# Kernel optimization log

Hardware: AMD Instinct MI355X
Metric: run time of the kernel (lower is better)

The kernel has to match this reference:

```python
import jax, jax.numpy as jnp
import numpy as np

N_GENES = 768
HID = 128


def setup_inputs() -> dict:
    key = jax.random.key(0)
    ks = jax.random.split(key, 7)
    s1 = 1.0 / np.sqrt(2 * HID)
    s2 = 1.0 / np.sqrt(HID)
    return {
        "gene_embeddings": jax.random.normal(ks[0], (N_GENES, HID), jnp.float32),
        # regulatory_classifier: Linear(2h -> h), ReLU, Linear(h -> 3)
        "W1": jax.random.normal(ks[1], (HID, 2 * HID), jnp.float32) * s1,
        "b1": jax.random.normal(ks[2], (HID,), jnp.float32) * s1,
        "W2": jax.random.normal(ks[3], (3, HID), jnp.float32) * s2,
        "b2": jax.random.normal(ks[4], (3,), jnp.float32) * s2,
        # binding_predictor: Bilinear(h, h, 1) -> weight [1, h, h], bias [1]
        "Wb": jax.random.normal(ks[5], (1, HID, HID), jnp.float32) * s2,
        "bb": jax.random.normal(ks[6], (1,), jnp.float32) * s2,
    }


def reference(gene_embeddings, W1, b1, W2, b2, Wb, bb):
    """Vectorized equivalent of GeneRegulatoryNetwork.compute_regulatory_matrix.

    For every ordered pair (i, j), i != j:
      logits   = MLP(cat[x_i, x_j])            -> [3]
      cls      = argmax(logits)
      affinity = x_i^T Wb x_j + bb             (nn.Bilinear, out=1)
      reg[i,j] = +affinity if cls==0, -affinity if cls==2, else 0
    """
    X = gene_embeddings  # [n, h]
    n, h = X.shape
    # Linear(2h -> h) on cat[x_i, x_j] splits into two per-gene projections.
    Ai = X @ W1[:, :h].T  # [n, h] contribution of gene_i
    Bj = X @ W1[:, h:].T  # [n, h] contribution of gene_j
    hidden = jax.nn.relu(Ai[:, None, :] + Bj[None, :, :] + b1)  # [n, n, h]
    logits = hidden @ W2.T + b2  # [n, n, 3]
    reg_class = jnp.argmax(logits, axis=-1)  # [n, n] (first-max, matches torch)
    # Bilinear affinity: x_i^T Wb[0] x_j + bb[0]
    affinity = jnp.einsum('ik,kl,jl->ij', X, Wb[0], X) + bb[0]  # [n, n]
    sign = jnp.where(reg_class == 0, 1.0, jnp.where(reg_class == 2, -1.0, 0.0))
    reg = (sign * affinity).astype(X.dtype)
    # i == j pairs are skipped in the original loop -> zero diagonal
    reg = reg * (1.0 - jnp.eye(n, dtype=reg.dtype))
    return reg
```

## Files before the change

### kernel.cpp

```cpp
#include <hip/hip_runtime.h>

#define N_GENES 768
#define H 128
#define TILE 48
#define LDP 132

__global__ __launch_bounds__(128) void grn_pre(
    const float* __restrict__ X, const float* __restrict__ W1,
    const float* __restrict__ b1, const float* __restrict__ Wb,
    float* __restrict__ AiB, float* __restrict__ Bjp, float* __restrict__ Y)
{
    const int m  = threadIdx.x;
    const int g0 = blockIdx.x * 4;

    __shared__ float Xs[4][H];
    #pragma unroll
    for (int r = 0; r < 4; ++r) Xs[r][m] = X[(g0 + r) * H + m];
    __syncthreads();

    double aib[4] = {0, 0, 0, 0}, bj[4] = {0, 0, 0, 0}, y[4] = {0, 0, 0, 0};
    const float4* W1a = (const float4*)(W1 + m * (2 * H));
    const float4* W1b = (const float4*)(W1 + m * (2 * H) + H);

    #pragma unroll 4
    for (int kq = 0; kq < H / 4; ++kq) {
        float4 wa = W1a[kq];
        float4 wb = W1b[kq];
        float wc[4];
        #pragma unroll
        for (int e = 0; e < 4; ++e) wc[e] = Wb[(kq * 4 + e) * H + m];
        const float* wae = &wa.x;
        const float* wbe = &wb.x;
        #pragma unroll
        for (int r = 0; r < 4; ++r) {
            float4 xr = *(const float4*)&Xs[r][kq * 4];
            const float* xe = &xr.x;
            #pragma unroll
            for (int e = 0; e < 4; ++e) {
                aib[r] += (double)xe[e] * (double)wae[e];
                bj[r]  += (double)xe[e] * (double)wbe[e];
                y[r]   += (double)xe[e] * (double)wc[e];
            }
        }
    }

    const double b1m = (double)b1[m];
    #pragma unroll
    for (int r = 0; r < 4; ++r) {
        AiB[(g0 + r) * H + m] = (float)(aib[r] + b1m);
        Bjp[(g0 + r) * H + m] = (float)bj[r];
        Y  [(g0 + r) * H + m] = (float)y[r];
    }
}

__device__ __forceinline__ void load_tile(float* __restrict__ dst,
                                          const float* __restrict__ src, int tx)
{
    #pragma unroll
    for (int t = 0; t < 6; ++t) {
        int idx = tx + t * 256;
        int row = idx >> 5;
        int c4  = idx & 31;
        *(float4*)&dst[row * LDP + c4 * 4] = *(const float4*)&src[row * H + c4 * 4];
    }
}

__global__ __launch_bounds__(256) void grn_main(
    const float* __restrict__ AiB, const float* __restrict__ Bjp,
    const float* __restrict__ Y,   const float* __restrict__ X,
    const float* __restrict__ W2,  const float* __restrict__ b2,
    const float* __restrict__ bb,  float* __restrict__ out)
{
    const int gj = blockIdx.x & 15;
    const int gi = blockIdx.x >> 4;
    const int tx = threadIdx.x;
    const int it = tx >> 4;
    const int jt = tx & 15;

    __shared__ float sL[TILE * LDP];
    __shared__ float sR[TILE * LDP];
    __shared__ float sW0[H];
    __shared__ float sW1[H];

    load_tile(sL, Y + gi * TILE * H, tx);
    load_tile(sR, X + gj * TILE * H, tx);
    if (tx < H) {
        sW0[tx] = W2[tx] - W2[2 * H + tx];
        sW1[tx] = W2[tx] - W2[H + tx];
    }
    __syncthreads();

    float aff[3][3] = {};
    #pragma unroll 4
    for (int mq = 0; mq < H / 4; ++mq) {
        float4 yv[3], xv[3];
        #pragma unroll
        for (int r = 0; r < 3; ++r) yv[r] = *(const float4*)&sL[(it + 16 * r) * LDP + mq * 4];
        #pragma unroll
        for (int c = 0; c < 3; ++c) xv[c] = *(const float4*)&sR[(jt + 16 * c) * LDP + mq * 4];
        #pragma unroll
        for (int r = 0; r < 3; ++r) {
            const float* ye = &yv[r].x;
            #pragma unroll
            for (int c = 0; c < 3; ++c) {
                const float* xe = &xv[c].x;
                #pragma unroll
                for (int e = 0; e < 4; ++e)
                    aff[r][c] = fmaf(ye[e], xe[e], aff[r][c]);
            }
        }
    }

    __syncthreads();

    load_tile(sL, AiB + gi * TILE * H, tx);
    load_tile(sR, Bjp + gj * TILE * H, tx);
    __syncthreads();

    const float u0 = b2[0] - b2[2];
    const float v0 = b2[0] - b2[1];
    float u[3][3], v[3][3];
    #pragma unroll
    for (int r = 0; r < 3; ++r)
        #pragma unroll
        for (int c = 0; c < 3; ++c) { u[r][c] = u0; v[r][c] = v0; }

    #pragma unroll 4
    for (int mq = 0; mq < H / 4; ++mq) {
        float4 w0 = *(const float4*)&sW0[mq * 4];
        float4 w1 = *(const float4*)&sW1[mq * 4];
        const float* w0e = &w0.x;
        const float* w1e = &w1.x;
        float4 av[3], bv[3];
        #pragma unroll
        for (int r = 0; r < 3; ++r) av[r] = *(const float4*)&sL[(it + 16 * r) * LDP + mq * 4];
        #pragma unroll
        for (int c = 0; c < 3; ++c) bv[c] = *(const float4*)&sR[(jt + 16 * c) * LDP + mq * 4];
        #pragma unroll
        for (int r = 0; r < 3; ++r) {
            const float* ae = &av[r].x;
            #pragma unroll
            for (int c = 0; c < 3; ++c) {
                const float* be = &bv[c].x;
                #pragma unroll
                for (int e = 0; e < 4; ++e) {
                    float h = fmaxf(ae[e] + be[e], 0.0f);
                    u[r][c] = fmaf(h, w0e[e], u[r][c]);
                    v[r][c] = fmaf(h, w1e[e], v[r][c]);
                }
            }
        }
    }

    const float bbv = bb[0];
    #pragma unroll
    for (int r = 0; r < 3; ++r) {
        const int i = gi * TILE + it + 16 * r;
        #pragma unroll
        for (int c = 0; c < 3; ++c) {
            const int j = gj * TILE + jt + 16 * c;
            float A = aff[r][c] + bbv;
            float uu = u[r][c], vv = v[r][c];
            float s = (uu >= 0.0f && vv >= 0.0f) ? A
                    : ((uu < 0.0f && uu < vv) ? -A : 0.0f);
            if (i == j) s = 0.0f;
            out[i * N_GENES + j] = s;
        }
    }
}

extern "C" void kernel_launch(void* const* d_in, const int* in_sizes, int n_in,
                              void* d_out, int out_size, void* d_ws, size_t ws_size,
                              hipStream_t stream)
{
    const float* X  = (const float*)d_in[0];
    const float* W1 = (const float*)d_in[1];
    const float* b1 = (const float*)d_in[2];
    const float* W2 = (const float*)d_in[3];
    const float* b2 = (const float*)d_in[4];
    const float* Wb = (const float*)d_in[5];
    const float* bb = (const float*)d_in[6];
    float* out = (float*)d_out;

    float* ws  = (float*)d_ws;
    float* AiB = ws;
    float* Bjp = ws + N_GENES * H;
    float* Yw  = ws + 2 * N_GENES * H;

    grn_pre <<<N_GENES / 4, 128, 0, stream>>>(X, W1, b1, Wb, AiB, Bjp, Yw);
    grn_main<<<256,         256, 0, stream>>>(AiB, Bjp, Yw, X, W2, b2, bb, out);
}
```

Before: 94.05 us.

## Compute bilinear affinity in fp16 with fdot2 and rebalance pre-kernel grid

The pre-kernel now writes the Y projection and a copy of X as fp16. The main kernel computes the bilinear affinity from these with packed fp16 dot-product instructions (fdot2), which halves the shared-memory and global traffic for that phase. The pre-kernel handles 3 genes per block instead of 4, giving more blocks, and the hidden-layer loop is rewritten with 2-wide vector add/max. The fp16 inputs lose precision in the affinity values, which may push results past the tolerance.

```diff
diff --git a/kernel.cpp b/kernel.cpp
--- a/kernel.cpp
+++ b/kernel.cpp
@@ -4,21 +4,27 @@
 #define H 128
 #define TILE 48
 #define LDP 132
+#define LDPH 136
+
+typedef float    f2 __attribute__((ext_vector_type(2)));
+typedef _Float16 h2 __attribute__((ext_vector_type(2)));
+typedef _Float16 h8 __attribute__((ext_vector_type(8)));
 
 __global__ __launch_bounds__(128) void grn_pre(
     const float* __restrict__ X, const float* __restrict__ W1,
     const float* __restrict__ b1, const float* __restrict__ Wb,
-    float* __restrict__ AiB, float* __restrict__ Bjp, float* __restrict__ Y)
+    float* __restrict__ AiB, float* __restrict__ Bjp,
+    _Float16* __restrict__ Yh, _Float16* __restrict__ Xh)
 {
     const int m  = threadIdx.x;
-    const int g0 = blockIdx.x * 4;
-
-    __shared__ float Xs[4][H];
-    #pragma unroll
-    for (int r = 0; r < 4; ++r) Xs[r][m] = X[(g0 + r) * H + m];
-    __syncthreads();
-
-    double aib[4] = {0, 0, 0, 0}, bj[4] = {0, 0, 0, 0}, y[4] = {0, 0, 0, 0};
+    const int g0 = blockIdx.x * 3;
+
+    __shared__ float Xs[3][H];
+    #pragma unroll
+    for (int r = 0; r < 3; ++r) Xs[r][m] = X[(g0 + r) * H + m];
+    __syncthreads();
+
+    double aib[3] = {0, 0, 0}, bj[3] = {0, 0, 0}, y[3] = {0, 0, 0};
     const float4* W1a = (const float4*)(W1 + m * (2 * H));
     const float4* W1b = (const float4*)(W1 + m * (2 * H) + H);
 
@@ -32,7 +38,7 @@
         const float* wae = &wa.x;
         const float* wbe = &wb.x;
         #pragma unroll
-        for (int r = 0; r < 4; ++r) {
+        for (int r = 0; r < 3; ++r) {
             float4 xr = *(const float4*)&Xs[r][kq * 4];
             const float* xe = &xr.x;
             #pragma unroll
@@ -46,15 +52,16 @@
 
     const double b1m = (double)b1[m];
     #pragma unroll
-    for (int r = 0; r < 4; ++r) {
+    for (int r = 0; r < 3; ++r) {
         AiB[(g0 + r) * H + m] = (float)(aib[r] + b1m);
         Bjp[(g0 + r) * H + m] = (float)bj[r];
-        Y  [(g0 + r) * H + m] = (float)y[r];
-    }
-}
-
-__device__ __forceinline__ void load_tile(float* __restrict__ dst,
-                                          const float* __restrict__ src, int tx)
+        Yh [(g0 + r) * H + m] = (_Float16)(float)y[r];
+        Xh [(g0 + r) * H + m] = (_Float16)Xs[r][m];
+    }
+}
+
+__device__ __forceinline__ void load_tile_f32(float* __restrict__ dst,
+                                              const float* __restrict__ src, int tx)
 {
     #pragma unroll
     for (int t = 0; t < 6; ++t) {
@@ -65,9 +72,23 @@
     }
 }
 
+__device__ __forceinline__ void load_tile_f16(_Float16* __restrict__ dst,
+                                              const _Float16* __restrict__ src, int tx)
+{
+    #pragma unroll
+    for (int t = 0; t < 3; ++t) {
+        int idx = tx + t * 256;
+        int row = idx >> 4;
+        int c8  = idx & 15;
+        *(h8*)&dst[row * LDPH + c8 * 8] = *(const h8*)&src[row * H + c8 * 8];
+    }
+}
+
+__device__ __forceinline__ h2 hpair(h8 v, int p) { h2 r; r.x = v[2*p]; r.y = v[2*p+1]; return r; }
+
 __global__ __launch_bounds__(256) void grn_main(
     const float* __restrict__ AiB, const float* __restrict__ Bjp,
-    const float* __restrict__ Y,   const float* __restrict__ X,
+    const _Float16* __restrict__ Yh, const _Float16* __restrict__ Xh,
     const float* __restrict__ W2,  const float* __restrict__ b2,
     const float* __restrict__ bb,  float* __restrict__ out)
 {
@@ -79,42 +100,48 @@
 
     __shared__ float sL[TILE * LDP];
     __shared__ float sR[TILE * LDP];
-    __shared__ float sW0[H];
-    __shared__ float sW1[H];
-
-    load_tile(sL, Y + gi * TILE * H, tx);
-    load_tile(sR, X + gj * TILE * H, tx);
+    __shared__ float sW[2 * H];
+
+    _Float16* sLh = (_Float16*)sL;
+    _Float16* sRh = (_Float16*)sR;
+
+    load_tile_f16(sLh, Yh + gi * TILE * H, tx);
+    load_tile_f16(sRh, Xh + gj * TILE * H, tx);
     if (tx < H) {
-        sW0[tx] = W2[tx] - W2[2 * H + tx];
-        sW1[tx] = W2[tx] - W2[H + tx];
+        sW[tx]     = W2[tx] - W2[2 * H + tx];
+        sW[H + tx] = W2[tx] - W2[H + tx];
     }
     __syncthreads();
 
     float aff[3][3] = {};
-    #pragma unroll 4
-    for (int mq = 0; mq < H / 4; ++mq) {
-        float4 yv[3], xv[3];
-        #pragma unroll
-        for (int r = 0; r < 3; ++r) yv[r] = *(const float4*)&sL[(it + 16 * r) * LDP + mq * 4];
-        #pragma unroll
-        for (int c = 0; c < 3; ++c) xv[c] = *(const float4*)&sR[(jt + 16 * c) * LDP + mq * 4];
-        #pragma unroll
-        for (int r = 0; r < 3; ++r) {
-            const float* ye = &yv[r].x;
+    #pragma unroll 2
+    for (int q = 0; q < H / 8; ++q) {
+        h8 yv[3], xv[3];
+        #pragma unroll
+        for (int r = 0; r < 3; ++r) yv[r] = *(const h8*)&sLh[(it + 16 * r) * LDPH + q * 8];
+        #pragma unroll
+        for (int c = 0; c < 3; ++c) xv[c] = *(const h8*)&sRh[(jt + 16 * c) * LDPH + q * 8];
+        #pragma unroll
+        for (int r = 0; r < 3; ++r)
             #pragma unroll
-            for (int c = 0; c < 3; ++c) {
-                const float* xe = &xv[c].x;
+            for (int c = 0; c < 3; ++c)
                 #pragma unroll
-                for (int e = 0; e < 4; ++e)
-                    aff[r][c] = fmaf(ye[e], xe[e], aff[r][c]);
-            }
-        }
-    }
-
-    __syncthreads();
-
-    load_tile(sL, AiB + gi * TILE * H, tx);
-    load_tile(sR, Bjp + gj * TILE * H, tx);
+                for (int p = 0; p < 4; ++p) {
+#if __has_builtin(__builtin_amdgcn_fdot2)
+                    aff[r][c] = __builtin_amdgcn_fdot2(hpair(yv[r], p), hpair(xv[c], p),
+                                                       aff[r][c], false);
+#else
+                    h2 a = hpair(yv[r], p), b = hpair(xv[c], p);
+                    aff[r][c] = fmaf((float)a.x, (float)b.x, aff[r][c]);
+                    aff[r][c] = fmaf((float)a.y, (float)b.y, aff[r][c]);
+#endif
+                }
+    }
+
+    __syncthreads();
+
+    load_tile_f32(sL, AiB + gi * TILE * H, tx);
+    load_tile_f32(sR, Bjp + gj * TILE * H, tx);
     __syncthreads();
 
     const float u0 = b2[0] - b2[2];
@@ -125,12 +152,11 @@
         #pragma unroll
         for (int c = 0; c < 3; ++c) { u[r][c] = u0; v[r][c] = v0; }
 
+    const f2 zero2 = {0.0f, 0.0f};
     #pragma unroll 4
     for (int mq = 0; mq < H / 4; ++mq) {
-        float4 w0 = *(const float4*)&sW0[mq * 4];
-        float4 w1 = *(const float4*)&sW1[mq * 4];
-        const float* w0e = &w0.x;
-        const float* w1e = &w1.x;
+        float4 w0 = *(const float4*)&sW[mq * 4];
+        float4 w1 = *(const float4*)&sW[H + mq * 4];
         float4 av[3], bv[3];
         #pragma unroll
         for (int r = 0; r < 3; ++r) av[r] = *(const float4*)&sL[(it + 16 * r) * LDP + mq * 4];
@@ -138,16 +164,20 @@
         for (int c = 0; c < 3; ++c) bv[c] = *(const float4*)&sR[(jt + 16 * c) * LDP + mq * 4];
         #pragma unroll
         for (int r = 0; r < 3; ++r) {
-            const float* ae = &av[r].x;
+            f2 a01 = {av[r].x, av[r].y};
+            f2 a23 = {av[r].z, av[r].w};
             #pragma unroll
             for (int c = 0; c < 3; ++c) {
-                const float* be = &bv[c].x;
-                #pragma unroll
-                for (int e = 0; e < 4; ++e) {
-                    float h = fmaxf(ae[e] + be[e], 0.0f);
-                    u[r][c] = fmaf(h, w0e[e], u[r][c]);
-                    v[r][c] = fmaf(h, w1e[e], v[r][c]);
-                }
+                f2 b01 = {bv[c].x, bv[c].y};
+                f2 b23 = {bv[c].z, bv[c].w};
+                f2 h01 = __builtin_elementwise_max(a01 + b01, zero2);
+                f2 h23 = __builtin_elementwise_max(a23 + b23, zero2);
+                float uu = u[r][c], vv = v[r][c];
+                uu = fmaf(h01.x, w0.x, uu); vv = fmaf(h01.x, w1.x, vv);
+                uu = fmaf(h01.y, w0.y, uu); vv = fmaf(h01.y, w1.y, vv);
+                uu = fmaf(h23.x, w0.z, uu); vv = fmaf(h23.x, w1.z, vv);
+                uu = fmaf(h23.y, w0.w, uu); vv = fmaf(h23.y, w1.w, vv);
+                u[r][c] = uu; v[r][c] = vv;
             }
         }
     }
@@ -183,10 +213,11 @@
     float* out = (float*)d_out;
 
     float* ws  = (float*)d_ws;
-    float* AiB = ws;
-    float* Bjp = ws + N_GENES * H;
-    float* Yw  = ws + 2 * N_GENES * H;
-
-    grn_pre <<<N_GENES / 4, 128, 0, stream>>>(X, W1, b1, Wb, AiB, Bjp, Yw);
-    grn_main<<<256,         256, 0, stream>>>(AiB, Bjp, Yw, X, W2, b2, bb, out);
-}
+    float*     AiB = ws;
+    float*     Bjp = ws + N_GENES * H;
+    _Float16*  Yh  = (_Float16*)(ws + 2 * N_GENES * H);
+    _Float16*  Xh  = (_Float16*)(ws + 2 * N_GENES * H) + N_GENES * H;
+
+    grn_pre <<<N_GENES / 3, 128, 0, stream>>>(X, W1, b1, Wb, AiB, Bjp, Yh, Xh);
+    grn_main<<<256,         256, 0, stream>>>(AiB, Bjp, Yh, Xh, W2, b2, bb, out);
+}
```

Result: faster. 88.33 us (-6.1%).
